# Performance work log

Measured on AMD Instinct MI355X. Metric: run time of the kernel, lower is better.

The kernel has to match this reference:

```python
import jax, jax.numpy as jnp
import numpy as np

B, L, E, H = 2, 2048, 1024, 16
D = E // H  # head_dim = 64


def setup_inputs() -> dict:
    key = jax.random.key(0)
    ks = jax.random.split(key, 9)
    s = 1.0 / np.sqrt(E)
    return {
        "query": jax.random.normal(ks[0], (B, L, E), jnp.float32),
        "key": jax.random.normal(ks[1], (B, L, E), jnp.float32),
        "value": jax.random.normal(ks[2], (B, L, E), jnp.float32),
        # torch Linear weights are [out_features, in_features]
        "Wq": jax.random.uniform(ks[3], (E, E), jnp.float32, -s, s),
        "bq": jnp.zeros((E,), jnp.float32),
        "Wk": jax.random.uniform(ks[4], (E, E), jnp.float32, -s, s),  # k_proj, no bias (add_bias_kv=False)
        "Wv": jax.random.uniform(ks[5], (E, E), jnp.float32, -s, s),  # v_proj, no bias
        "Wo": jax.random.uniform(ks[6], (E, E), jnp.float32, -s, s),
        "bo": jnp.zeros((E,), jnp.float32),
    }


def reference(query, key, value, Wq, bq, Wk, Wv, Wo, bo):
    # Projections (torch Linear: y = x @ W.T + b)
    q = query @ Wq.T + bq          # [B, L, E]
    k = key @ Wk.T                 # [B, L, E]
    v = value @ Wv.T               # [B, L, E]
    # Split heads
    q = q.reshape(B, L, H, D)
    k = k.reshape(B, L, H, D)
    v = v.reshape(B, L, H, D)
    # Scaled dot-product attention; the source's chunked online-softmax
    # computes exactly softmax(q k^T / sqrt(D)) v.
    q = q / jnp.sqrt(jnp.asarray(D, q.dtype))
    scores = jnp.einsum("bqhd,bkhd->bhqk", q, k)      # [B, H, L, L]
    probs = jax.nn.softmax(scores, axis=-1)
    out = jnp.einsum("bhqk,bkhd->bqhd", probs, v)     # [B, L, H, D]
    out = out.reshape(B, L, E)
    return out @ Wo.T + bo
```

## Files before the change

kernel.cpp:

```cpp
#include <hip/hip_runtime.h>

typedef __bf16 bf16;
typedef __bf16 bf16x8 __attribute__((ext_vector_type(8)));
typedef __bf16 bf16x4 __attribute__((ext_vector_type(4)));
typedef float  f32x4  __attribute__((ext_vector_type(4)));

#define MFMA_BF16(a, b, c) __builtin_amdgcn_mfma_f32_16x16x32_bf16((a), (b), (c), 0, 0, 0)


__device__ __forceinline__ void async_load16(const bf16* g, const bf16* l) {
    auto gp = (const __attribute__((address_space(1))) unsigned int*)(unsigned long long)(const void*)g;
    auto lp = (__attribute__((address_space(3))) unsigned int*)(unsigned int)(unsigned long long)(const void*)l;
    __builtin_amdgcn_global_load_lds(gp, lp, 16, 0, 0);
}

__global__ void cvt_bf16_kernel(
    const float* __restrict__ s0, const float* __restrict__ s1, const float* __restrict__ s2,
    const float* __restrict__ s3, const float* __restrict__ s4, const float* __restrict__ s5,
    const float* __restrict__ s6,
    bf16* __restrict__ d0, bf16* __restrict__ d1, bf16* __restrict__ d2,
    bf16* __restrict__ d3, bf16* __restrict__ d4, bf16* __restrict__ d5,
    bf16* __restrict__ d6)
{
    const float* src; bf16* dst; int n;
    switch (blockIdx.y) {
        case 0: src = s0; dst = d0; n = 4194304; break;
        case 1: src = s1; dst = d1; n = 4194304; break;
        case 2: src = s2; dst = d2; n = 4194304; break;
        case 3: src = s3; dst = d3; n = 1048576; break;
        case 4: src = s4; dst = d4; n = 1048576; break;
        case 5: src = s5; dst = d5; n = 1048576; break;
        default: src = s6; dst = d6; n = 1048576; break;
    }
    int i = (blockIdx.x * 256 + threadIdx.x) * 4;
    if (i >= n) return;
    float4 f = *(const float4*)(src + i);
    bf16x4 o;
    o.x = (bf16)f.x; o.y = (bf16)f.y; o.z = (bf16)f.z; o.w = (bf16)f.w;
    *(bf16x4*)(dst + i) = o;
}

__global__ __launch_bounds__(256, 2) void gemm4_kernel(
    const bf16* __restrict__ Aq, const bf16* __restrict__ Ak, const bf16* __restrict__ Av,
    const bf16* __restrict__ Ao,
    const bf16* __restrict__ Wq, const bf16* __restrict__ Wk, const bf16* __restrict__ Wv,
    const bf16* __restrict__ Wo,
    const float* __restrict__ bq, const float* __restrict__ bo,
    bf16* __restrict__ Qs, bf16* __restrict__ Ksw, bf16* __restrict__ Vsw,
    float* __restrict__ out, int zbase)
{
    const int z = zbase + blockIdx.z;
    const bf16 *A, *W;
    if (z == 0)      { A = Aq; W = Wq; }
    else if (z == 1) { A = Ak; W = Wk; }
    else if (z == 2) { A = Av; W = Wv; }
    else             { A = Ao; W = Wo; }

    __shared__ __align__(16) bf16 lA[128 * 32];
    __shared__ __align__(16) bf16 lB[128 * 32];

    const int tid  = threadIdx.x;
    const int w    = tid >> 6;
    const int lane = tid & 63;
    const int lm   = lane & 15;
    const int g    = lane >> 4;
    const int m0   = blockIdx.y * 128;
    const int n0   = blockIdx.x * 128;
    const int wm   = (w & 1) * 64;
    const int wn   = (w >> 1) * 64;

    f32x4 acc[4][4] = {};
    const int sbase = w * 128 + lane;

    for (int kb = 0; kb < 32; kb++) {
        __syncthreads();
#pragma unroll
        for (int t = 0; t < 2; t++) {
            int s   = sbase + t * 64;
            int row = s >> 2;
            int gs  = s & 3;
            int gg  = gs ^ ((row >> 1) & 3);
            const bf16* ga = A + (size_t)(m0 + row) * 1024 + kb * 32 + gg * 8;
            const bf16* gb = W + (size_t)(n0 + row) * 1024 + kb * 32 + gg * 8;
            async_load16(ga, lA + s * 8);
            async_load16(gb, lB + s * 8);
        }
        __syncthreads();

        bf16x8 af[4], bfr[4];
#pragma unroll
        for (int mt = 0; mt < 4; mt++) {
            int row = wm + mt * 16 + lm;
            af[mt] = *(const bf16x8*)(lA + row * 32 + ((g ^ ((row >> 1) & 3)) << 3));
        }
#pragma unroll
        for (int nt = 0; nt < 4; nt++) {
            int row = wn + nt * 16 + lm;
            bfr[nt] = *(const bf16x8*)(lB + row * 32 + ((g ^ ((row >> 1) & 3)) << 3));
        }
#pragma unroll
        for (int mt = 0; mt < 4; mt++)
#pragma unroll
            for (int nt = 0; nt < 4; nt++)
                acc[mt][nt] = MFMA_BF16(af[mt], bfr[nt], acc[mt][nt]);
    }

    const float scale = (z == 0) ? 0.18033688011112042f : 1.0f;
    const float* bias = (z == 0) ? bq : ((z == 3) ? bo : nullptr);
#pragma unroll
    for (int nt = 0; nt < 4; nt++) {
        int n = n0 + wn + nt * 16 + lm;
        float bv = bias ? bias[n] : 0.0f;
#pragma unroll
        for (int mt = 0; mt < 4; mt++) {
#pragma unroll
            for (int r = 0; r < 4; r++) {
                int m = m0 + wm + mt * 16 + g * 4 + r;
                float val = (acc[mt][nt][r] + bv) * scale;
                if (z == 3) {
                    out[(size_t)m * 1024 + n] = val;
                } else {
                    int b = m >> 11, lpos = m & 2047, h = n >> 6, d = n & 63;
                    size_t hb = (size_t)(b * 16 + h) * (2048 * 64);
                    if (z == 0) {
                        Qs[hb + (size_t)lpos * 64 + d] = (bf16)val;
                    } else if (z == 1) {
                        int kb2 = lpos >> 6, rem = lpos & 63;
                        int c   = ((rem >> 4) & 2) | ((rem >> 2) & 1);
                        int lmk = ((rem >> 1) & 12) | (rem & 3);
                        int f   = d >> 5, gk = (d >> 3) & 3, j = d & 7;
                        Ksw[hb + (size_t)((kb2 * 8 + c * 2 + f) * 64 + gk * 16 + lmk) * 8 + j] = (bf16)val;
                    } else {
                        int kb2 = lpos >> 6, kc = (lpos >> 5) & 1, gv = (lpos >> 3) & 3, j = lpos & 7;
                        int mt2 = d >> 4, lmv = d & 15;
                        Vsw[hb + (size_t)((kb2 * 8 + mt2 * 2 + kc) * 64 + gv * 16 + lmv) * 8 + j] = (bf16)val;
                    }
                }
            }
        }
    }
}

__global__ __launch_bounds__(128, 4) void attn_kernel(
    const bf16* __restrict__ Qs, const bf16* __restrict__ Ksw,
    const bf16* __restrict__ Vsw, bf16* __restrict__ attn)
{
    const int w    = threadIdx.x >> 6;
    const int lane = threadIdx.x & 63;
    const int lm   = lane & 15;
    const int g    = lane >> 4;
    const int i    = blockIdx.x;
    const int bh   = ((i & 7) << 2) | ((i >> 3) & 3);
    const int q0   = (i >> 5) * 32;

    const bf16* Qh = Qs  + (size_t)bh * (2048 * 64);
    const bf16* kp = Ksw + (size_t)bh * (2048 * 64) + (size_t)(w * 16) * 4096 + (size_t)lane * 8;
    const bf16* vp = Vsw + (size_t)bh * (2048 * 64) + (size_t)(w * 16) * 4096 + (size_t)lane * 8;

    bf16x8 qf[2][2];
#pragma unroll
    for (int qi = 0; qi < 2; qi++)
#pragma unroll
        for (int f = 0; f < 2; f++)
            qf[qi][f] = *(const bf16x8*)(Qh + (size_t)(q0 + qi * 16 + lm) * 64 + f * 32 + g * 8);

    bf16x8 ones;
#pragma unroll
    for (int j = 0; j < 8; j++) ones[j] = (bf16)1.0f;

    f32x4 o[2][4] = {};
    f32x4 lacc[2] = {};

    bf16x8 kf[4][2];
#pragma unroll
    for (int c = 0; c < 4; c++)
#pragma unroll
        for (int f = 0; f < 2; f++)
            kf[c][f] = *(const bf16x8*)(kp + (c * 2 + f) * 512);

    for (int kb = 0; kb < 16; kb++) {
        f32x4 s[2][4] = {};
#pragma unroll
        for (int c = 0; c < 4; c++)
#pragma unroll
            for (int f = 0; f < 2; f++) {
                s[0][c] = MFMA_BF16(kf[c][f], qf[0][f], s[0][c]);
                s[1][c] = MFMA_BF16(kf[c][f], qf[1][f], s[1][c]);
            }

        bf16x8 vf[4][2];
#pragma unroll
        for (int mt = 0; mt < 4; mt++)
#pragma unroll
            for (int kc = 0; kc < 2; kc++)
                vf[mt][kc] = *(const bf16x8*)(vp + (mt * 2 + kc) * 512);
        vp += 4096;

        kp += 4096;
        if (kb < 15) {
#pragma unroll
            for (int c = 0; c < 4; c++)
#pragma unroll
                for (int f = 0; f < 2; f++)
                    kf[c][f] = *(const bf16x8*)(kp + (c * 2 + f) * 512);
        }

        bf16x8 pb[2][2];
#pragma unroll
        for (int qi = 0; qi < 2; qi++)
#pragma unroll
            for (int kc = 0; kc < 2; kc++)
#pragma unroll
                for (int r = 0; r < 4; r++) {
                    pb[qi][kc][r]     = (bf16)exp2f(s[qi][2 * kc][r]);
                    pb[qi][kc][r + 4] = (bf16)exp2f(s[qi][2 * kc + 1][r]);
                }

#pragma unroll
        for (int kc = 0; kc < 2; kc++) {
            lacc[0] = MFMA_BF16(ones, pb[0][kc], lacc[0]);
            lacc[1] = MFMA_BF16(ones, pb[1][kc], lacc[1]);
#pragma unroll
            for (int mt = 0; mt < 4; mt++) {
                o[0][mt] = MFMA_BF16(vf[mt][kc], pb[0][kc], o[0][mt]);
                o[1][mt] = MFMA_BF16(vf[mt][kc], pb[1][kc], o[1][mt]);
            }
        }
    }

    __shared__ float part[64 * 36];
    if (w == 1) {
        float* p = part + lane * 36;
#pragma unroll
        for (int qi = 0; qi < 2; qi++)
#pragma unroll
            for (int mt = 0; mt < 4; mt++)
                *(f32x4*)(p + (qi * 4 + mt) * 4) = o[qi][mt];
        p[32] = lacc[0][0];
        p[33] = lacc[1][0];
    }
    __syncthreads();
    if (w == 0) {
        const float* p = part + lane * 36;
#pragma unroll
        for (int qi = 0; qi < 2; qi++)
#pragma unroll
            for (int mt = 0; mt < 4; mt++) {
                f32x4 t = *(const f32x4*)(p + (qi * 4 + mt) * 4);
#pragma unroll
                for (int r = 0; r < 4; r++) o[qi][mt][r] += t[r];
            }
        float ltot0 = lacc[0][0] + p[32];
        float ltot1 = lacc[1][0] + p[33];

        const int b = bh >> 4, h = bh & 15;
#pragma unroll
        for (int qi = 0; qi < 2; qi++) {
            float inv = 1.0f / (qi == 0 ? ltot0 : ltot1);
            bf16* orow = attn + ((size_t)(b * 2048 + q0 + qi * 16 + lm)) * 1024 + h * 64;
#pragma unroll
            for (int mt = 0; mt < 4; mt++) {
                bf16x4 ov;
#pragma unroll
                for (int r = 0; r < 4; r++) ov[r] = (bf16)(o[qi][mt][r] * inv);
                *(bf16x4*)(orow + mt * 16 + g * 4) = ov;
            }
        }
    }
}

extern "C" void kernel_launch(void* const* d_in, const int* in_sizes, int n_in,
                              void* d_out, int out_size, void* d_ws, size_t ws_size,
                              hipStream_t stream) {
    const float* query = (const float*)d_in[0];
    const float* key   = (const float*)d_in[1];
    const float* value = (const float*)d_in[2];
    const float* Wq    = (const float*)d_in[3];
    const float* bq    = (const float*)d_in[4];
    const float* Wk    = (const float*)d_in[5];
    const float* Wv    = (const float*)d_in[6];
    const float* Wo    = (const float*)d_in[7];
    const float* bo    = (const float*)d_in[8];

    char* ws = (char*)d_ws;
    bf16* Xq  = (bf16*)(ws);
    bf16* Xk  = (bf16*)(ws + ((size_t)8  << 20));
    bf16* Xv  = (bf16*)(ws + ((size_t)16 << 20));
    bf16* Wqb = (bf16*)(ws + ((size_t)24 << 20));
    bf16* Wkb = (bf16*)(ws + ((size_t)26 << 20));
    bf16* Wvb = (bf16*)(ws + ((size_t)28 << 20));
    bf16* Wob = (bf16*)(ws + ((size_t)30 << 20));
    bf16* Qs  = (bf16*)(ws + ((size_t)32 << 20));
    bf16* Ksw = (bf16*)(ws + ((size_t)40 << 20));
    bf16* Vsw = (bf16*)(ws + ((size_t)48 << 20));
    bf16* attn = Xq;

    cvt_bf16_kernel<<<dim3(4096, 7, 1), 256, 0, stream>>>(
        query, key, value, Wq, Wk, Wv, Wo, Xq, Xk, Xv, Wqb, Wkb, Wvb, Wob);

    gemm4_kernel<<<dim3(8, 32, 3), 256, 0, stream>>>(
        Xq, Xk, Xv, attn, Wqb, Wkb, Wvb, Wob, bq, bo, Qs, Ksw, Vsw, (float*)d_out, 0);

    attn_kernel<<<dim3(2048, 1, 1), 128, 0, stream>>>(Qs, Ksw, Vsw, attn);

    gemm4_kernel<<<dim3(8, 32, 1), 256, 0, stream>>>(
        Xq, Xk, Xv, attn, Wqb, Wkb, Wvb, Wob, bq, bo, Qs, Ksw, Vsw, (float*)d_out, 3);
}
```

Measured before the change: 241.1 us.

## Transpose GEMM operands for vectorized epilogue stores and retile output projection

The projection GEMMs now swap the A/B operand roles per output (weights as A for Q, K and the output projection; activations as A for V). This makes each lane's four accumulator rows map to contiguous destination elements, so epilogue writes become bf16x4/f32x4 vector stores instead of scalar scattered stores. The output projection uses a templated 128x64 tile with more blocks and a higher occupancy hint. The attention kernel initializes its score MFMA with zero, uses the raw hardware exp2, and stages the output through LDS so global writes are coalesced 16-byte rows. The risks are a more complex index mapping and the cost of the extra LDS staging.

Result: faster. 214.8 us (-10.9%).

```diff
diff --git a/kernel.cpp b/kernel.cpp
--- a/kernel.cpp
+++ b/kernel.cpp
@@ -40,8 +40,9 @@
     *(bf16x4*)(dst + i) = o;
 }
 
-__global__ __launch_bounds__(256, 2) void gemm4_kernel(
-    const bf16* __restrict__ Aq, const bf16* __restrict__ Ak, const bf16* __restrict__ Av,
+template<int BN>
+__global__ __launch_bounds__(256, (BN == 128) ? 2 : 4) void gemm4_kernel(
+    const bf16* __restrict__ Xq, const bf16* __restrict__ Xk, const bf16* __restrict__ Xv,
     const bf16* __restrict__ Ao,
     const bf16* __restrict__ Wq, const bf16* __restrict__ Wk, const bf16* __restrict__ Wv,
     const bf16* __restrict__ Wo,
@@ -50,92 +51,136 @@
     float* __restrict__ out, int zbase)
 {
     const int z = zbase + blockIdx.z;
-    const bf16 *A, *W;
-    if (z == 0)      { A = Aq; W = Wq; }
-    else if (z == 1) { A = Ak; W = Wk; }
-    else if (z == 2) { A = Av; W = Wv; }
-    else             { A = Ao; W = Wo; }
+    const bf16 *Amat, *Bmat;
+    if (z == 0)      { Amat = Wq; Bmat = Xq; }
+    else if (z == 1) { Amat = Wk; Bmat = Xk; }
+    else if (z == 2) { Amat = Xv; Bmat = Wv; }
+    else             { Amat = Wo; Bmat = Ao; }
+
+    const int m0 = (z == 2 ? blockIdx.y : blockIdx.x) * 128;
+    const int n0 = (z == 2 ? blockIdx.x : blockIdx.y) * BN;
 
     __shared__ __align__(16) bf16 lA[128 * 32];
-    __shared__ __align__(16) bf16 lB[128 * 32];
+    __shared__ __align__(16) bf16 lB[BN * 32];
 
     const int tid  = threadIdx.x;
     const int w    = tid >> 6;
     const int lane = tid & 63;
     const int lm   = lane & 15;
     const int g    = lane >> 4;
-    const int m0   = blockIdx.y * 128;
-    const int n0   = blockIdx.x * 128;
     const int wm   = (w & 1) * 64;
-    const int wn   = (w >> 1) * 64;
-
-    f32x4 acc[4][4] = {};
-    const int sbase = w * 128 + lane;
+    const int wn   = (w >> 1) * (BN / 2);
+    constexpr int NT = BN / 32;
+    constexpr int T  = (128 + BN) / 64;
+
+    f32x4 acc[4][NT] = {};
 
     for (int kb = 0; kb < 32; kb++) {
         __syncthreads();
 #pragma unroll
-        for (int t = 0; t < 2; t++) {
-            int s   = sbase + t * 64;
+        for (int t = 0; t < T; t++) {
+            int s   = (t * 4 + w) * 64 + lane;
             int row = s >> 2;
             int gs  = s & 3;
             int gg  = gs ^ ((row >> 1) & 3);
-            const bf16* ga = A + (size_t)(m0 + row) * 1024 + kb * 32 + gg * 8;
-            const bf16* gb = W + (size_t)(n0 + row) * 1024 + kb * 32 + gg * 8;
-            async_load16(ga, lA + s * 8);
-            async_load16(gb, lB + s * 8);
+            if (row < 128)
+                async_load16(Amat + (size_t)(m0 + row) * 1024 + kb * 32 + gg * 8, lA + s * 8);
+            else
+                async_load16(Bmat + (size_t)(n0 + row - 128) * 1024 + kb * 32 + gg * 8,
+                             lB + (s - 512) * 8);
         }
         __syncthreads();
 
-        bf16x8 af[4], bfr[4];
+        bf16x8 af[4], bfr[NT];
 #pragma unroll
         for (int mt = 0; mt < 4; mt++) {
             int row = wm + mt * 16 + lm;
             af[mt] = *(const bf16x8*)(lA + row * 32 + ((g ^ ((row >> 1) & 3)) << 3));
         }
 #pragma unroll
-        for (int nt = 0; nt < 4; nt++) {
+        for (int nt = 0; nt < NT; nt++) {
             int row = wn + nt * 16 + lm;
             bfr[nt] = *(const bf16x8*)(lB + row * 32 + ((g ^ ((row >> 1) & 3)) << 3));
         }
 #pragma unroll
         for (int mt = 0; mt < 4; mt++)
 #pragma unroll
-            for (int nt = 0; nt < 4; nt++)
+            for (int nt = 0; nt < NT; nt++)
                 acc[mt][nt] = MFMA_BF16(af[mt], bfr[nt], acc[mt][nt]);
     }
 
-    const float scale = (z == 0) ? 0.18033688011112042f : 1.0f;
-    const float* bias = (z == 0) ? bq : ((z == 3) ? bo : nullptr);
-#pragma unroll
-    for (int nt = 0; nt < 4; nt++) {
-        int n = n0 + wn + nt * 16 + lm;
-        float bv = bias ? bias[n] : 0.0f;
-#pragma unroll
-        for (int mt = 0; mt < 4; mt++) {
-#pragma unroll
-            for (int r = 0; r < 4; r++) {
-                int m = m0 + wm + mt * 16 + g * 4 + r;
-                float val = (acc[mt][nt][r] + bv) * scale;
-                if (z == 3) {
-                    out[(size_t)m * 1024 + n] = val;
-                } else {
-                    int b = m >> 11, lpos = m & 2047, h = n >> 6, d = n & 63;
-                    size_t hb = (size_t)(b * 16 + h) * (2048 * 64);
-                    if (z == 0) {
-                        Qs[hb + (size_t)lpos * 64 + d] = (bf16)val;
-                    } else if (z == 1) {
-                        int kb2 = lpos >> 6, rem = lpos & 63;
-                        int c   = ((rem >> 4) & 2) | ((rem >> 2) & 1);
-                        int lmk = ((rem >> 1) & 12) | (rem & 3);
-                        int f   = d >> 5, gk = (d >> 3) & 3, j = d & 7;
-                        Ksw[hb + (size_t)((kb2 * 8 + c * 2 + f) * 64 + gk * 16 + lmk) * 8 + j] = (bf16)val;
-                    } else {
-                        int kb2 = lpos >> 6, kc = (lpos >> 5) & 1, gv = (lpos >> 3) & 3, j = lpos & 7;
-                        int mt2 = d >> 4, lmv = d & 15;
-                        Vsw[hb + (size_t)((kb2 * 8 + mt2 * 2 + kc) * 64 + gv * 16 + lmv) * 8 + j] = (bf16)val;
-                    }
-                }
+    if (z == 3) {
+#pragma unroll
+        for (int mt = 0; mt < 4; mt++) {
+            int mb = m0 + wm + mt * 16 + g * 4;
+            f32x4 bov = *(const f32x4*)(bo + mb);
+#pragma unroll
+            for (int nt = 0; nt < NT; nt++) {
+                int n = n0 + wn + nt * 16 + lm;
+                f32x4 val;
+#pragma unroll
+                for (int r = 0; r < 4; r++) val[r] = acc[mt][nt][r] + bov[r];
+                *(f32x4*)(out + (size_t)n * 1024 + mb) = val;
+            }
+        }
+    } else if (z == 2) {
+#pragma unroll
+        for (int mt = 0; mt < 4; mt++) {
+            int mb   = m0 + wm + mt * 16 + g * 4;
+            int b    = mb >> 11;
+            int lpos = mb & 2047;
+            int kb2  = lpos >> 6, kc = (lpos >> 5) & 1, gv = (lpos >> 3) & 3, j0 = lpos & 7;
+#pragma unroll
+            for (int nt = 0; nt < NT; nt++) {
+                int n = n0 + wn + nt * 16 + lm;
+                int h = n >> 6, mt2 = (n >> 4) & 3, lmv = n & 15;
+                bf16x4 ov;
+#pragma unroll
+                for (int r = 0; r < 4; r++) ov[r] = (bf16)acc[mt][nt][r];
+                *(bf16x4*)(Vsw + (size_t)(b * 16 + h) * 131072 +
+                           (size_t)((kb2 * 8 + mt2 * 2 + kc) * 64 + gv * 16 + lmv) * 8 + j0) = ov;
+            }
+        }
+    } else if (z == 1) {
+#pragma unroll
+        for (int mt = 0; mt < 4; mt++) {
+            int mb = m0 + wm + mt * 16 + g * 4;
+            int h  = mb >> 6;
+            int f  = (mb >> 5) & 1, gk = (mb >> 3) & 3, j0 = mb & 7;
+#pragma unroll
+            for (int nt = 0; nt < NT; nt++) {
+                int n    = n0 + wn + nt * 16 + lm;
+                int b    = n >> 11;
+                int lpos = n & 2047;
+                int kb2  = lpos >> 6;
+                int rem  = lpos & 63;
+                int c    = ((rem >> 4) & 2) | ((rem >> 2) & 1);
+                int lmk  = ((rem >> 1) & 12) | (rem & 3);
+                bf16x4 ov;
+#pragma unroll
+                for (int r = 0; r < 4; r++) ov[r] = (bf16)acc[mt][nt][r];
+                *(bf16x4*)(Ksw + (size_t)(b * 16 + h) * 131072 +
+                           (size_t)((kb2 * 8 + c * 2 + f) * 64 + gk * 16 + lmk) * 8 + j0) = ov;
+            }
+        }
+    } else {
+        const float qscale = 0.18033688011112042f;
+#pragma unroll
+        for (int mt = 0; mt < 4; mt++) {
+            int mb  = m0 + wm + mt * 16 + g * 4;
+            int h   = mb >> 6;
+            int dd0 = mb & 63;
+            f32x4 bqv = *(const f32x4*)(bq + mb);
+#pragma unroll
+            for (int nt = 0; nt < NT; nt++) {
+                int n    = n0 + wn + nt * 16 + lm;
+                int b    = n >> 11;
+                int lpos = n & 2047;
+                bf16x4 ov;
+#pragma unroll
+                for (int r = 0; r < 4; r++)
+                    ov[r] = (bf16)((acc[mt][nt][r] + bqv[r]) * qscale);
+                *(bf16x4*)(Qs + (size_t)((b * 16 + h) * 2048 + lpos) * 64 + dd0) = ov;
             }
         }
     }
@@ -167,6 +212,7 @@
     bf16x8 ones;
 #pragma unroll
     for (int j = 0; j < 8; j++) ones[j] = (bf16)1.0f;
+    const f32x4 fzero = {0.0f, 0.0f, 0.0f, 0.0f};
 
     f32x4 o[2][4] = {};
     f32x4 lacc[2] = {};
@@ -179,14 +225,14 @@
             kf[c][f] = *(const bf16x8*)(kp + (c * 2 + f) * 512);
 
     for (int kb = 0; kb < 16; kb++) {
-        f32x4 s[2][4] = {};
-#pragma unroll
-        for (int c = 0; c < 4; c++)
-#pragma unroll
-            for (int f = 0; f < 2; f++) {
-                s[0][c] = MFMA_BF16(kf[c][f], qf[0][f], s[0][c]);
-                s[1][c] = MFMA_BF16(kf[c][f], qf[1][f], s[1][c]);
-            }
+        f32x4 s[2][4];
+#pragma unroll
+        for (int c = 0; c < 4; c++) {
+            s[0][c] = MFMA_BF16(kf[c][0], qf[0][0], fzero);
+            s[1][c] = MFMA_BF16(kf[c][0], qf[1][0], fzero);
+            s[0][c] = MFMA_BF16(kf[c][1], qf[0][1], s[0][c]);
+            s[1][c] = MFMA_BF16(kf[c][1], qf[1][1], s[1][c]);
+        }
 
         bf16x8 vf[4][2];
 #pragma unroll
@@ -212,8 +258,8 @@
             for (int kc = 0; kc < 2; kc++)
 #pragma unroll
                 for (int r = 0; r < 4; r++) {
-                    pb[qi][kc][r]     = (bf16)exp2f(s[qi][2 * kc][r]);
-                    pb[qi][kc][r + 4] = (bf16)exp2f(s[qi][2 * kc + 1][r]);
+                    pb[qi][kc][r]     = (bf16)__builtin_amdgcn_exp2f(s[qi][2 * kc][r]);
+                    pb[qi][kc][r + 4] = (bf16)__builtin_amdgcn_exp2f(s[qi][2 * kc + 1][r]);
                 }
 
 #pragma unroll
@@ -229,6 +275,7 @@
     }
 
     __shared__ float part[64 * 36];
+    __shared__ __align__(16) bf16 ost[32 * 72];
     if (w == 1) {
         float* p = part + lane * 36;
 #pragma unroll
@@ -250,21 +297,27 @@
 #pragma unroll
                 for (int r = 0; r < 4; r++) o[qi][mt][r] += t[r];
             }
-        float ltot0 = lacc[0][0] + p[32];
-        float ltot1 = lacc[1][0] + p[33];
-
-        const int b = bh >> 4, h = bh & 15;
+        float inv0 = 1.0f / (lacc[0][0] + p[32]);
+        float inv1 = 1.0f / (lacc[1][0] + p[33]);
+
 #pragma unroll
         for (int qi = 0; qi < 2; qi++) {
-            float inv = 1.0f / (qi == 0 ? ltot0 : ltot1);
-            bf16* orow = attn + ((size_t)(b * 2048 + q0 + qi * 16 + lm)) * 1024 + h * 64;
+            float inv = qi ? inv1 : inv0;
 #pragma unroll
             for (int mt = 0; mt < 4; mt++) {
                 bf16x4 ov;
 #pragma unroll
                 for (int r = 0; r < 4; r++) ov[r] = (bf16)(o[qi][mt][r] * inv);
-                *(bf16x4*)(orow + mt * 16 + g * 4) = ov;
-            }
+                *(bf16x4*)(ost + (qi * 16 + lm) * 72 + mt * 16 + g * 4) = ov;
+            }
+        }
+        const int b = bh >> 4, h = bh & 15;
+#pragma unroll
+        for (int it = 0; it < 4; it++) {
+            int cc = it * 64 + lane;
+            int q  = cc >> 3, ch = cc & 7;
+            bf16x8 t = *(const bf16x8*)(ost + q * 72 + ch * 8);
+            *(bf16x8*)(attn + (size_t)(b * 2048 + q0 + q) * 1024 + h * 64 + ch * 8) = t;
         }
     }
 }
@@ -298,11 +351,11 @@
     cvt_bf16_kernel<<<dim3(4096, 7, 1), 256, 0, stream>>>(
         query, key, value, Wq, Wk, Wv, Wo, Xq, Xk, Xv, Wqb, Wkb, Wvb, Wob);
 
-    gemm4_kernel<<<dim3(8, 32, 3), 256, 0, stream>>>(
+    gemm4_kernel<128><<<dim3(8, 32, 3), 256, 0, stream>>>(
         Xq, Xk, Xv, attn, Wqb, Wkb, Wvb, Wob, bq, bo, Qs, Ksw, Vsw, (float*)d_out, 0);
 
     attn_kernel<<<dim3(2048, 1, 1), 128, 0, stream>>>(Qs, Ksw, Vsw, attn);
 
-    gemm4_kernel<<<dim3(8, 32, 1), 256, 0, stream>>>(
+    gemm4_kernel<64><<<dim3(8, 64, 1), 256, 0, stream>>>(
         Xq, Xk, Xv, attn, Wqb, Wkb, Wvb, Wob, bq, bo, Qs, Ksw, Vsw, (float*)d_out, 3);
 }
```
